# Kernel tuning notes

Measured on AMD Instinct MI355X. Metric: run time of the kernel, lower is better.

## Reference

```python
import jax, jax.numpy as jnp
import numpy as np

N_HEADS = 16

def setup_inputs() -> dict:
    key = jax.random.key(0)
    ks = jax.random.split(key, 5)
    B, T, D, L = 2, 2048, 1024, 128
    x = jax.random.normal(ks[0], (B, T, D), dtype=jnp.float32)
    w_q = jax.random.normal(ks[1], (D, D), dtype=jnp.float32) / np.sqrt(D)
    w_d = jax.random.normal(ks[2], (D, L), dtype=jnp.float32) / np.sqrt(D)
    w_k = jax.random.normal(ks[3], (L, D), dtype=jnp.float32) / np.sqrt(L)
    w_v = jax.random.normal(ks[4], (L, D), dtype=jnp.float32) / np.sqrt(L)
    mask = jnp.ones((B, T), dtype=jnp.int32)
    return {"x": x, "mask": mask, "w_q": w_q, "w_d": w_d, "w_k": w_k, "w_v": w_v}


def reference(x, mask, w_q, w_d, w_k, w_v):
    B, T, D = x.shape
    H = N_HEADS
    dh = D // H
    q = x @ w_q                      # [B,T,D]
    latent = x @ w_d                 # [B,T,L]
    k = latent @ w_k                 # [B,T,D]
    v = latent @ w_v                 # [B,T,D]

    def split(t):
        return t.reshape(B, T, H, dh).transpose(0, 2, 1, 3)  # [B,H,T,dh]

    q, k, v = split(q), split(k), split(v)
    scores = jnp.einsum('bhqd,bhkd->bhqk', q, k) / jnp.sqrt(jnp.float32(dh))
    causal = jnp.tril(jnp.ones((T, T), dtype=bool))          # [T,T]
    keep = causal[None, None, :, :] & (mask[:, None, None, :] != 0)
    scores = jnp.where(keep, scores, jnp.float32(-jnp.inf))
    probs = jax.nn.softmax(scores, axis=-1)
    out = jnp.einsum('bhqk,bhkd->bhqd', probs, v)            # [B,H,T,dh]
    return out.transpose(0, 2, 1, 3).reshape(B, T, D)
```

## Files before the change

kernel.cpp:

```cpp
#include <hip/hip_runtime.h>

typedef __attribute__((ext_vector_type(8))) short bf16x8;
typedef __attribute__((ext_vector_type(4))) float f32x4;
typedef __attribute__((ext_vector_type(4))) unsigned u32x4;

__device__ inline unsigned short f2bf(float f) {
  unsigned u = __builtin_bit_cast(unsigned, f);
  unsigned r = u + 0x7FFFu + ((u >> 16) & 1u);
  return (unsigned short)(r >> 16);
}
__device__ inline float bf2f(unsigned short s) {
  unsigned u = ((unsigned)s) << 16;
  return __builtin_bit_cast(float, u);
}
__device__ inline float fexp2(float x) { return __builtin_amdgcn_exp2f(x); }

__device__ inline void gload_lds16(const unsigned short* g, unsigned short* l) {
  __builtin_amdgcn_global_load_lds(
      (const __attribute__((address_space(1))) unsigned int*)g,
      (__attribute__((address_space(3))) unsigned int*)l, 16, 0, 0);
}

__device__ __host__ inline int pv_perm(int k) {
  return ((k >> 5) & 1) * 32 + ((k >> 2) & 3) * 8 + ((k >> 4) & 1) * 4 + (k & 3);
}

__global__ __launch_bounds__(256) void prep_kernel(
    const float* __restrict__ x, const int* __restrict__ mask,
    const float* __restrict__ w_q, const float* __restrict__ w_d,
    const float* __restrict__ w_k, const float* __restrict__ w_v,
    unsigned short* __restrict__ x_bf, unsigned short* __restrict__ wqdt,
    unsigned short* __restrict__ wkvt, float* __restrict__ bias,
    int* __restrict__ tileok) {
  int bid = blockIdx.x;
  if (bid < 1024) {
    int base = bid * 4096 + threadIdx.x * 4;
#pragma unroll
    for (int it = 0; it < 4; ++it) {
      int idx = base + it * 1024;
      float4 v = *(const float4*)&x[idx];
      ushort4 o;
      o.x = f2bf(v.x); o.y = f2bf(v.y); o.z = f2bf(v.z); o.w = f2bf(v.w);
      *(ushort4*)&x_bf[idx] = o;
    }
    return;
  }
  int tb = bid - 1024;
  if (tb >= 1408) {
    int i = (tb - 1408) * 256 + threadIdx.x;
    int mv = mask[i];
    bias[i] = mv ? 0.0f : -1e30f;
    int ok = __all(mv != 0);
    if ((threadIdx.x & 63) == 0) tileok[i >> 6] = ok;
    return;
  }
  const float* in; unsigned short* out; int R, C, tr, tc;
  if (tb < 1024)      { in = w_q; out = wqdt;               R = 1024; C = 1024; tr = tb >> 5; tc = tb & 31; }
  else if (tb < 1152) { int t2 = tb - 1024; in = w_d; out = wqdt + 1024 * 1024; R = 1024; C = 128; tr = t2 >> 2; tc = t2 & 3; }
  else if (tb < 1280) { int t2 = tb - 1152; in = w_k; out = wkvt;               R = 128; C = 1024; tr = t2 >> 5; tc = t2 & 31; }
  else                { int t2 = tb - 1280; in = w_v; out = wkvt + 1024 * 128;  R = 128; C = 1024; tr = t2 >> 5; tc = t2 & 31; }
  __shared__ float t[32][33];
  int r0 = tr * 32, c0 = tc * 32;
  int tx = threadIdx.x & 31, ty = threadIdx.x >> 5;
  for (int r = ty; r < 32; r += 8)
    t[r][tx] = in[(size_t)(r0 + r) * C + c0 + tx];
  __syncthreads();
  for (int cc = ty; cc < 32; cc += 8)
    out[(size_t)(c0 + cc) * R + r0 + tx] = f2bf(t[tx][cc]);
}

__global__ __launch_bounds__(256) void vt_kernel(const unsigned short* __restrict__ kv,
                                                 unsigned short* __restrict__ vt) {
  int bh = blockIdx.x, tt = blockIdx.y, dt = blockIdx.z;
  int b = bh >> 4, h = bh & 15;
  __shared__ unsigned short tile[32][33];
  int tx = threadIdx.x & 31, ty = threadIdx.x >> 5;
  for (int r = ty; r < 32; r += 8)
    tile[r][tx] = kv[(size_t)(b * 2048 + tt * 32 + r) * 2048 + 1024 + h * 64 + dt * 32 + tx];
  __syncthreads();
  int tile64 = tt >> 1;
  int wbase = (tt & 1) * 32;
  for (int r = ty; r < 32; r += 8) {
    int kp = pv_perm(wbase + tx);
    vt[((size_t)(bh * 64 + dt * 32 + r)) * 2048 + tile64 * 64 + kp] = tile[tx][r];
  }
}

template <int BN>
__global__ __launch_bounds__(256) void gemm_bt(const unsigned short* __restrict__ A, int lda,
                                               const unsigned short* __restrict__ Bt, int ldb,
                                               unsigned short* __restrict__ C, int ldc,
                                               int K) {
  constexpr int WM = (BN == 128) ? 2 : 4;
  constexpr int WN = 4 / WM;
  constexpr int MR = 128 / WM / 16;
  constexpr int NR = BN / WN / 16;
  constexpr int RPW = 128 / WM;
  constexpr int CPW = BN / WN;
  __shared__ unsigned short As[128 * 32];
  __shared__ unsigned short Bs[BN * 32];
  int m0 = blockIdx.x * 128, n0 = blockIdx.y * BN;
  int tid = threadIdx.x, w = tid >> 6, l = tid & 63;
  int lr = l & 15, lg = l >> 4;
  int wr = w / WN, wc = w % WN;
  f32x4 acc[MR][NR] = {};

  for (int k0 = 0; k0 < K; k0 += 32) {
    __syncthreads();
#pragma unroll
    for (int it = 0; it < 2; ++it) {
      int c = w * 2 + it;
      int row = c * 16 + (l >> 2);
      int col = (l & 3) * 8;
      gload_lds16(&A[(size_t)(m0 + row) * lda + k0 + col], &As[c * 512 + l * 8]);
    }
    if constexpr (BN == 128) {
#pragma unroll
      for (int it = 0; it < 2; ++it) {
        int c = w * 2 + it;
        int row = c * 16 + (l >> 2);
        int col = (l & 3) * 8;
        gload_lds16(&Bt[(size_t)(n0 + row) * ldb + k0 + col], &Bs[c * 512 + l * 8]);
      }
    } else {
      int row = w * 16 + (l >> 2);
      int col = (l & 3) * 8;
      gload_lds16(&Bt[(size_t)(n0 + row) * ldb + k0 + col], &Bs[w * 512 + l * 8]);
    }
    __syncthreads();
    bf16x8 af[MR], bfr[NR];
#pragma unroll
    for (int m = 0; m < MR; ++m)
      af[m] = *(const bf16x8*)&As[(wr * RPW + m * 16 + lr) * 32 + lg * 8];
#pragma unroll
    for (int n = 0; n < NR; ++n)
      bfr[n] = *(const bf16x8*)&Bs[(wc * CPW + n * 16 + lr) * 32 + lg * 8];
    __builtin_amdgcn_s_setprio(1);
#pragma unroll
    for (int m = 0; m < MR; ++m)
#pragma unroll
      for (int n = 0; n < NR; ++n)
        acc[m][n] = __builtin_amdgcn_mfma_f32_16x16x32_bf16(af[m], bfr[n], acc[m][n], 0, 0, 0);
    __builtin_amdgcn_s_setprio(0);
  }

#pragma unroll
  for (int m = 0; m < MR; ++m)
#pragma unroll
    for (int n = 0; n < NR; ++n)
#pragma unroll
      for (int i = 0; i < 4; ++i)
        C[(size_t)(m0 + wr * RPW + m * 16 + lg * 4 + i) * ldc + n0 + wc * CPW + n * 16 + lr] =
            f2bf(acc[m][n][i]);
}

__global__ __launch_bounds__(128, 4) void attn_kernel(const unsigned short* __restrict__ qg,
                                                      const unsigned short* __restrict__ kvg,
                                                      const unsigned short* __restrict__ vtg,
                                                      const float* __restrict__ biasg,
                                                      const int* __restrict__ tileokg,
                                                      float* __restrict__ outg) {
  const int bh = blockIdx.x, qt32 = 63 - blockIdx.y;
  const int b = bh >> 4, h = bh & 15;
  const int tid = threadIdx.x, w = tid >> 6, l = tid & 63;
  const int lr = l & 15, lg = l >> 4;

  __shared__ unsigned short Ks[64 * 72];
  __shared__ unsigned short Vs[64 * 72];

  const int qrow0 = qt32 * 32 + w * 16;
  const int nkv = (qt32 >> 1) + 1;
  const int diagoff = (qt32 & 1) * 32 + w * 16 + lr;
  const float QSCALE = 0.125f * 1.44269504089f;

  bf16x8 qf[2];
#pragma unroll
  for (int s = 0; s < 2; ++s) {
    bf16x8 raw = *(const bf16x8*)&qg[(size_t)(b * 2048 + qrow0 + lr) * 1152 + h * 64 + s * 32 + lg * 8];
#pragma unroll
    for (int j = 0; j < 8; ++j)
      raw[j] = (short)f2bf(bf2f((unsigned short)raw[j]) * QSCALE);
    qf[s] = raw;
  }

  f32x4 acc[4] = {};
  float m_i = -1e30f;
  float l_part = 0.f;

  bf16x8 kreg[4], vreg[4];
#pragma unroll
  for (int it = 0; it < 4; ++it) {
    int slot = it * 128 + tid, row = slot >> 3, c8 = (slot & 7) * 8;
    kreg[it] = *(const bf16x8*)&kvg[(size_t)(b * 2048 + row) * 2048 + h * 64 + c8];
    vreg[it] = *(const bf16x8*)&vtg[((size_t)(bh * 64 + row)) * 2048 + c8];
  }
#pragma unroll
  for (int it = 0; it < 4; ++it) {
    int slot = it * 128 + tid, row = slot >> 3, c8 = (slot & 7) * 8;
    *(bf16x8*)&Ks[row * 72 + c8] = kreg[it];
    *(bf16x8*)&Vs[row * 72 + c8] = vreg[it];
  }
  __syncthreads();

  for (int kt = 0; kt < nkv; ++kt) {
    if (kt + 1 < nkv) {
#pragma unroll
      for (int it = 0; it < 4; ++it) {
        int slot = it * 128 + tid, row = slot >> 3, c8 = (slot & 7) * 8;
        kreg[it] = *(const bf16x8*)&kvg[(size_t)(b * 2048 + (kt + 1) * 64 + row) * 2048 + h * 64 + c8];
        vreg[it] = *(const bf16x8*)&vtg[((size_t)(bh * 64 + row)) * 2048 + (kt + 1) * 64 + c8];
      }
    }

    f32x4 s[4];
    __builtin_amdgcn_s_setprio(1);
#pragma unroll
    for (int n = 0; n < 4; ++n) {
      f32x4 z = {};
#pragma unroll
      for (int ks = 0; ks < 2; ++ks) {
        bf16x8 kf = *(const bf16x8*)&Ks[(n * 16 + lr) * 72 + ks * 32 + lg * 8];
        z = __builtin_amdgcn_mfma_f32_16x16x32_bf16(kf, qf[ks], z, 0, 0, 0);
      }
      s[n] = z;
    }
    __builtin_amdgcn_s_setprio(0);

    const int tok = tileokg[b * 32 + kt];
    const bool diag = (kt == nkv - 1);
    float p[4][4];
    float mx = -1e30f;
    if (tok) {
      if (diag) {
#pragma unroll
        for (int n = 0; n < 4; ++n)
#pragma unroll
          for (int i = 0; i < 4; ++i) {
            float v = (n * 16 + lg * 4 + i <= diagoff) ? s[n][i] : -1e30f;
            p[n][i] = v;
            mx = fmaxf(mx, v);
          }
      } else {
#pragma unroll
        for (int n = 0; n < 4; ++n)
#pragma unroll
          for (int i = 0; i < 4; ++i) {
            p[n][i] = s[n][i];
            mx = fmaxf(mx, s[n][i]);
          }
      }
    } else {
#pragma unroll
      for (int n = 0; n < 4; ++n)
#pragma unroll
        for (int i = 0; i < 4; ++i) {
          int keyl = n * 16 + lg * 4 + i;
          float v = s[n][i] + biasg[b * 2048 + kt * 64 + keyl];
          if (diag) v = (keyl <= diagoff) ? v : -1e30f;
          p[n][i] = v;
          mx = fmaxf(mx, v);
        }
    }
    mx = fmaxf(mx, __shfl_xor(mx, 16, 64));
    mx = fmaxf(mx, __shfl_xor(mx, 32, 64));

    if (__any(mx - m_i > 8.0f)) {
      float mn = fmaxf(m_i, mx);
      float sc = fexp2(m_i - mn);
      m_i = mn;
      l_part *= sc;
      float scb[4];
#pragma unroll
      for (int i = 0; i < 4; ++i) scb[i] = __shfl(sc, lg * 4 + i, 64);
#pragma unroll
      for (int dt = 0; dt < 4; ++dt)
#pragma unroll
        for (int i = 0; i < 4; ++i) acc[dt][i] *= scb[i];
    }

    float rs = 0.f;
#pragma unroll
    for (int n = 0; n < 4; ++n)
#pragma unroll
      for (int i = 0; i < 4; ++i) {
        float e = fexp2(p[n][i] - m_i);
        p[n][i] = e;
        rs += e;
      }
    l_part += rs;

    unsigned pk[4][2];
#pragma unroll
    for (int n = 0; n < 4; ++n) {
      asm("v_cvt_pk_bf16_f32 %0, %1, %2" : "=v"(pk[n][0]) : "v"(p[n][0]), "v"(p[n][1]));
      asm("v_cvt_pk_bf16_f32 %0, %1, %2" : "=v"(pk[n][1]) : "v"(p[n][2]), "v"(p[n][3]));
    }
    bf16x8 paf[2];
#pragma unroll
    for (int ks = 0; ks < 2; ++ks) {
      u32x4 uv;
      uv[0] = pk[2 * ks][0];
      uv[1] = pk[2 * ks][1];
      uv[2] = pk[2 * ks + 1][0];
      uv[3] = pk[2 * ks + 1][1];
      paf[ks] = __builtin_bit_cast(bf16x8, uv);
    }

    __builtin_amdgcn_s_setprio(1);
#pragma unroll
    for (int ks = 0; ks < 2; ++ks) {
#pragma unroll
      for (int dt = 0; dt < 4; ++dt) {
        bf16x8 vf = *(const bf16x8*)&Vs[(dt * 16 + lr) * 72 + ks * 32 + lg * 8];
        acc[dt] = __builtin_amdgcn_mfma_f32_16x16x32_bf16(paf[ks], vf, acc[dt], 0, 0, 0);
      }
    }
    __builtin_amdgcn_s_setprio(0);

    __syncthreads();
    if (kt + 1 < nkv) {
#pragma unroll
      for (int it = 0; it < 4; ++it) {
        int slot = it * 128 + tid, row = slot >> 3, c8 = (slot & 7) * 8;
        *(bf16x8*)&Ks[row * 72 + c8] = kreg[it];
        *(bf16x8*)&Vs[row * 72 + c8] = vreg[it];
      }
      __syncthreads();
    }
  }

  float lt = l_part;
  lt += __shfl_xor(lt, 16, 64);
  lt += __shfl_xor(lt, 32, 64);
  float inv = 1.f / lt;
  float invb[4];
#pragma unroll
  for (int i = 0; i < 4; ++i) invb[i] = __shfl(inv, lg * 4 + i, 64);
#pragma unroll
  for (int dt = 0; dt < 4; ++dt)
#pragma unroll
    for (int i = 0; i < 4; ++i)
      outg[(size_t)(b * 2048 + qrow0 + lg * 4 + i) * 1024 + h * 64 + dt * 16 + lr] =
          acc[dt][i] * invb[i];
}

extern "C" void kernel_launch(void* const* d_in, const int* in_sizes, int n_in,
                              void* d_out, int out_size, void* d_ws, size_t ws_size,
                              hipStream_t stream) {
  const float* x    = (const float*)d_in[0];
  const int*   mask = (const int*)d_in[1];
  const float* w_q  = (const float*)d_in[2];
  const float* w_d  = (const float*)d_in[3];
  const float* w_k  = (const float*)d_in[4];
  const float* w_v  = (const float*)d_in[5];
  float* out = (float*)d_out;

  char* ws = (char*)d_ws;
  size_t off = 0;
  auto alloc = [&](size_t elems) {
    unsigned short* p = (unsigned short*)(ws + off);
    off += ((elems * 2 + 255) & ~(size_t)255);
    return p;
  };
  unsigned short* x_bf = alloc(4194304);
  unsigned short* wqdt = alloc(1152 * 1024);
  unsigned short* wkvt = alloc(2048 * 128);
  unsigned short* qlat = alloc(4096 * 1152);
  unsigned short* kv   = alloc(4096 * 2048);
  unsigned short* vt   = alloc(4194304);
  float* bias = (float*)alloc(8192);
  int* tileok = (int*)alloc(128);

  prep_kernel<<<2448, 256, 0, stream>>>(x, mask, w_q, w_d, w_k, w_v, x_bf, wqdt, wkvt, bias, tileok);

  gemm_bt<64><<<dim3(32, 18), 256, 0, stream>>>(x_bf, 1024, wqdt, 1024, qlat, 1152, 1024);
  gemm_bt<128><<<dim3(32, 16), 256, 0, stream>>>(qlat + 1024, 1152, wkvt, 128, kv, 2048, 128);

  vt_kernel<<<dim3(32, 64, 2), 256, 0, stream>>>(kv, vt);
  attn_kernel<<<dim3(32, 64), 128, 0, stream>>>(qlat, kv, vt, bias, tileok, out);
}
```

Before: 89.08 us.

## Fuse V transpose into KV GEMM epilogue and restructure attention to single-wave register tiles

Removes the separate vt_kernel by having a new gemm_kv kernel write K normally and V directly in the permuted transposed layout from its epilogue, saving a launch and a round trip of V through memory. The attention kernel becomes one wave per block handling 32 query rows as two 16-row sub-blocks. K/V fragments are loaded straight from global memory into registers with prefetch, dropping the LDS staging and __syncthreads. This raises register pressure and exposes global load latency in exchange for no LDS traffic or barriers, with fewer waves per block.

```diff
diff --git a/kernel.cpp b/kernel.cpp
--- a/kernel.cpp
+++ b/kernel.cpp
@@ -67,23 +67,6 @@
   __syncthreads();
   for (int cc = ty; cc < 32; cc += 8)
     out[(size_t)(c0 + cc) * R + r0 + tx] = f2bf(t[tx][cc]);
-}
-
-__global__ __launch_bounds__(256) void vt_kernel(const unsigned short* __restrict__ kv,
-                                                 unsigned short* __restrict__ vt) {
-  int bh = blockIdx.x, tt = blockIdx.y, dt = blockIdx.z;
-  int b = bh >> 4, h = bh & 15;
-  __shared__ unsigned short tile[32][33];
-  int tx = threadIdx.x & 31, ty = threadIdx.x >> 5;
-  for (int r = ty; r < 32; r += 8)
-    tile[r][tx] = kv[(size_t)(b * 2048 + tt * 32 + r) * 2048 + 1024 + h * 64 + dt * 32 + tx];
-  __syncthreads();
-  int tile64 = tt >> 1;
-  int wbase = (tt & 1) * 32;
-  for (int r = ty; r < 32; r += 8) {
-    int kp = pv_perm(wbase + tx);
-    vt[((size_t)(bh * 64 + dt * 32 + r)) * 2048 + tile64 * 64 + kp] = tile[tx][r];
-  }
 }
 
 template <int BN>
@@ -154,100 +137,163 @@
             f2bf(acc[m][n][i]);
 }
 
-__global__ __launch_bounds__(128, 4) void attn_kernel(const unsigned short* __restrict__ qg,
-                                                      const unsigned short* __restrict__ kvg,
-                                                      const unsigned short* __restrict__ vtg,
-                                                      const float* __restrict__ biasg,
-                                                      const int* __restrict__ tileokg,
-                                                      float* __restrict__ outg) {
+__global__ __launch_bounds__(256) void gemm_kv(const unsigned short* __restrict__ A,
+                                               const unsigned short* __restrict__ Bt,
+                                               unsigned short* __restrict__ kvK,
+                                               unsigned short* __restrict__ vt) {
+  __shared__ unsigned short As[128 * 32];
+  __shared__ unsigned short Bs[128 * 32];
+  int m0 = blockIdx.x * 128, n0 = blockIdx.y * 128;
+  int tid = threadIdx.x, w = tid >> 6, l = tid & 63;
+  int lr = l & 15, lg = l >> 4;
+  int wr = w >> 1, wc = w & 1;
+  f32x4 acc[4][4] = {};
+
+  for (int k0 = 0; k0 < 128; k0 += 32) {
+    __syncthreads();
+#pragma unroll
+    for (int it = 0; it < 2; ++it) {
+      int c = w * 2 + it;
+      int row = c * 16 + (l >> 2);
+      int col = (l & 3) * 8;
+      gload_lds16(&A[(size_t)(m0 + row) * 1152 + k0 + col], &As[c * 512 + l * 8]);
+      gload_lds16(&Bt[(size_t)(n0 + row) * 128 + k0 + col], &Bs[c * 512 + l * 8]);
+    }
+    __syncthreads();
+    bf16x8 af[4], bfr[4];
+#pragma unroll
+    for (int m = 0; m < 4; ++m)
+      af[m] = *(const bf16x8*)&As[(wr * 64 + m * 16 + lr) * 32 + lg * 8];
+#pragma unroll
+    for (int n = 0; n < 4; ++n)
+      bfr[n] = *(const bf16x8*)&Bs[(wc * 64 + n * 16 + lr) * 32 + lg * 8];
+    __builtin_amdgcn_s_setprio(1);
+#pragma unroll
+    for (int m = 0; m < 4; ++m)
+#pragma unroll
+      for (int n = 0; n < 4; ++n)
+        acc[m][n] = __builtin_amdgcn_mfma_f32_16x16x32_bf16(af[m], bfr[n], acc[m][n], 0, 0, 0);
+    __builtin_amdgcn_s_setprio(0);
+  }
+
+  if (blockIdx.y < 8) {
+#pragma unroll
+    for (int m = 0; m < 4; ++m)
+#pragma unroll
+      for (int n = 0; n < 4; ++n)
+#pragma unroll
+        for (int i = 0; i < 4; ++i)
+          kvK[(size_t)(m0 + wr * 64 + m * 16 + lg * 4 + i) * 2048 + n0 + wc * 64 + n * 16 + lr] =
+              f2bf(acc[m][n][i]);
+  } else {
+#pragma unroll
+    for (int m = 0; m < 4; ++m)
+#pragma unroll
+      for (int n = 0; n < 4; ++n) {
+        int vc = n0 - 1024 + wc * 64 + n * 16 + lr;
+        int hh = vc >> 6, dd = vc & 63;
+        int row0 = m0 + wr * 64 + m * 16 + lg * 4;
+        int bb = row0 >> 11, t0 = row0 & 2047;
+        size_t vrow = (size_t)((bb * 16 + hh) * 64 + dd);
+        int slot = (t0 >> 6) * 64 + pv_perm(t0 & 63);
+        ushort4 o;
+        o.x = f2bf(acc[m][n][0]); o.y = f2bf(acc[m][n][1]);
+        o.z = f2bf(acc[m][n][2]); o.w = f2bf(acc[m][n][3]);
+        *(ushort4*)&vt[vrow * 2048 + slot] = o;
+      }
+  }
+}
+
+__global__ __launch_bounds__(64, 2) void attn_kernel(const unsigned short* __restrict__ qg,
+                                                     const unsigned short* __restrict__ kvg,
+                                                     const unsigned short* __restrict__ vtg,
+                                                     const float* __restrict__ biasg,
+                                                     const int* __restrict__ tileokg,
+                                                     float* __restrict__ outg) {
   const int bh = blockIdx.x, qt32 = 63 - blockIdx.y;
   const int b = bh >> 4, h = bh & 15;
-  const int tid = threadIdx.x, w = tid >> 6, l = tid & 63;
-  const int lr = l & 15, lg = l >> 4;
-
-  __shared__ unsigned short Ks[64 * 72];
-  __shared__ unsigned short Vs[64 * 72];
-
-  const int qrow0 = qt32 * 32 + w * 16;
+  const int l = threadIdx.x & 63, lr = l & 15, lg = l >> 4;
+  const int qrow0 = qt32 * 32;
   const int nkv = (qt32 >> 1) + 1;
-  const int diagoff = (qt32 & 1) * 32 + w * 16 + lr;
+  const int dov0 = (qt32 & 1) * 32 + lr;
   const float QSCALE = 0.125f * 1.44269504089f;
 
-  bf16x8 qf[2];
-#pragma unroll
-  for (int s = 0; s < 2; ++s) {
-    bf16x8 raw = *(const bf16x8*)&qg[(size_t)(b * 2048 + qrow0 + lr) * 1152 + h * 64 + s * 32 + lg * 8];
-#pragma unroll
-    for (int j = 0; j < 8; ++j)
-      raw[j] = (short)f2bf(bf2f((unsigned short)raw[j]) * QSCALE);
-    qf[s] = raw;
-  }
-
-  f32x4 acc[4] = {};
-  float m_i = -1e30f;
-  float l_part = 0.f;
-
-  bf16x8 kreg[4], vreg[4];
-#pragma unroll
-  for (int it = 0; it < 4; ++it) {
-    int slot = it * 128 + tid, row = slot >> 3, c8 = (slot & 7) * 8;
-    kreg[it] = *(const bf16x8*)&kvg[(size_t)(b * 2048 + row) * 2048 + h * 64 + c8];
-    vreg[it] = *(const bf16x8*)&vtg[((size_t)(bh * 64 + row)) * 2048 + c8];
-  }
-#pragma unroll
-  for (int it = 0; it < 4; ++it) {
-    int slot = it * 128 + tid, row = slot >> 3, c8 = (slot & 7) * 8;
-    *(bf16x8*)&Ks[row * 72 + c8] = kreg[it];
-    *(bf16x8*)&Vs[row * 72 + c8] = vreg[it];
-  }
-  __syncthreads();
+  bf16x8 qf[2][2];
+#pragma unroll
+  for (int qb = 0; qb < 2; ++qb)
+#pragma unroll
+    for (int ks = 0; ks < 2; ++ks) {
+      bf16x8 raw = *(const bf16x8*)&qg[(size_t)(b * 2048 + qrow0 + qb * 16 + lr) * 1152 +
+                                       h * 64 + ks * 32 + lg * 8];
+#pragma unroll
+      for (int j = 0; j < 8; ++j)
+        raw[j] = (short)f2bf(bf2f((unsigned short)raw[j]) * QSCALE);
+      qf[qb][ks] = raw;
+    }
+
+  const unsigned short* kptr = kvg + (size_t)(b * 2048 + lr) * 2048 + h * 64 + lg * 8;
+  const unsigned short* vptr = vtg + (size_t)(bh * 64 + lr) * 2048 + lg * 8;
+
+  bf16x8 kf[4][2], vf[4][2];
+#pragma unroll
+  for (int n = 0; n < 4; ++n)
+#pragma unroll
+    for (int ks = 0; ks < 2; ++ks) {
+      kf[n][ks] = *(const bf16x8*)(kptr + (size_t)(n * 16) * 2048 + ks * 32);
+      vf[n][ks] = *(const bf16x8*)(vptr + (size_t)(n * 16) * 2048 + ks * 32);
+    }
+
+  f32x4 acc[4][2] = {};
+  float m_i[2] = {-1e30f, -1e30f};
+  float l_part[2] = {0.f, 0.f};
 
   for (int kt = 0; kt < nkv; ++kt) {
+    f32x4 s[2][4];
+    __builtin_amdgcn_s_setprio(1);
+#pragma unroll
+    for (int qb = 0; qb < 2; ++qb)
+#pragma unroll
+      for (int n = 0; n < 4; ++n) {
+        f32x4 z = {};
+#pragma unroll
+        for (int ks = 0; ks < 2; ++ks)
+          z = __builtin_amdgcn_mfma_f32_16x16x32_bf16(kf[n][ks], qf[qb][ks], z, 0, 0, 0);
+        s[qb][n] = z;
+      }
+    __builtin_amdgcn_s_setprio(0);
+
     if (kt + 1 < nkv) {
 #pragma unroll
-      for (int it = 0; it < 4; ++it) {
-        int slot = it * 128 + tid, row = slot >> 3, c8 = (slot & 7) * 8;
-        kreg[it] = *(const bf16x8*)&kvg[(size_t)(b * 2048 + (kt + 1) * 64 + row) * 2048 + h * 64 + c8];
-        vreg[it] = *(const bf16x8*)&vtg[((size_t)(bh * 64 + row)) * 2048 + (kt + 1) * 64 + c8];
-      }
-    }
-
-    f32x4 s[4];
-    __builtin_amdgcn_s_setprio(1);
-#pragma unroll
-    for (int n = 0; n < 4; ++n) {
-      f32x4 z = {};
-#pragma unroll
-      for (int ks = 0; ks < 2; ++ks) {
-        bf16x8 kf = *(const bf16x8*)&Ks[(n * 16 + lr) * 72 + ks * 32 + lg * 8];
-        z = __builtin_amdgcn_mfma_f32_16x16x32_bf16(kf, qf[ks], z, 0, 0, 0);
-      }
-      s[n] = z;
-    }
-    __builtin_amdgcn_s_setprio(0);
+      for (int n = 0; n < 4; ++n)
+#pragma unroll
+        for (int ks = 0; ks < 2; ++ks)
+          kf[n][ks] = *(const bf16x8*)(kptr + (size_t)((kt + 1) * 64 + n * 16) * 2048 + ks * 32);
+    }
 
     const int tok = tileokg[b * 32 + kt];
     const bool diag = (kt == nkv - 1);
-    float p[4][4];
-    float mx = -1e30f;
+    float mx[2] = {-1e30f, -1e30f};
     if (tok) {
       if (diag) {
 #pragma unroll
-        for (int n = 0; n < 4; ++n)
-#pragma unroll
-          for (int i = 0; i < 4; ++i) {
-            float v = (n * 16 + lg * 4 + i <= diagoff) ? s[n][i] : -1e30f;
-            p[n][i] = v;
-            mx = fmaxf(mx, v);
-          }
+        for (int qb = 0; qb < 2; ++qb)
+#pragma unroll
+          for (int n = 0; n < 4; ++n)
+#pragma unroll
+            for (int i = 0; i < 4; ++i) {
+              int keyl = n * 16 + lg * 4 + i;
+              float v = (keyl <= dov0 + qb * 16) ? s[qb][n][i] : -1e30f;
+              s[qb][n][i] = v;
+              mx[qb] = fmaxf(mx[qb], v);
+            }
       } else {
 #pragma unroll
-        for (int n = 0; n < 4; ++n)
-#pragma unroll
-          for (int i = 0; i < 4; ++i) {
-            p[n][i] = s[n][i];
-            mx = fmaxf(mx, s[n][i]);
-          }
+        for (int qb = 0; qb < 2; ++qb)
+#pragma unroll
+          for (int n = 0; n < 4; ++n)
+#pragma unroll
+            for (int i = 0; i < 4; ++i)
+              mx[qb] = fmaxf(mx[qb], s[qb][n][i]);
       }
     } else {
 #pragma unroll
@@ -255,93 +301,104 @@
 #pragma unroll
         for (int i = 0; i < 4; ++i) {
           int keyl = n * 16 + lg * 4 + i;
-          float v = s[n][i] + biasg[b * 2048 + kt * 64 + keyl];
-          if (diag) v = (keyl <= diagoff) ? v : -1e30f;
-          p[n][i] = v;
-          mx = fmaxf(mx, v);
+          float bsv = biasg[b * 2048 + kt * 64 + keyl];
+#pragma unroll
+          for (int qb = 0; qb < 2; ++qb) {
+            float v = s[qb][n][i] + bsv;
+            if (diag) v = (keyl <= dov0 + qb * 16) ? v : -1e30f;
+            s[qb][n][i] = v;
+            mx[qb] = fmaxf(mx[qb], v);
+          }
         }
     }
-    mx = fmaxf(mx, __shfl_xor(mx, 16, 64));
-    mx = fmaxf(mx, __shfl_xor(mx, 32, 64));
-
-    if (__any(mx - m_i > 8.0f)) {
-      float mn = fmaxf(m_i, mx);
-      float sc = fexp2(m_i - mn);
-      m_i = mn;
-      l_part *= sc;
-      float scb[4];
-#pragma unroll
-      for (int i = 0; i < 4; ++i) scb[i] = __shfl(sc, lg * 4 + i, 64);
+#pragma unroll
+    for (int qb = 0; qb < 2; ++qb) {
+      mx[qb] = fmaxf(mx[qb], __shfl_xor(mx[qb], 16, 64));
+      mx[qb] = fmaxf(mx[qb], __shfl_xor(mx[qb], 32, 64));
+    }
+
+    float g = fmaxf(mx[0] - m_i[0], mx[1] - m_i[1]);
+    if (__any(g > 8.0f)) {
+#pragma unroll
+      for (int qb = 0; qb < 2; ++qb) {
+        float mn = fmaxf(m_i[qb], mx[qb]);
+        float sc = fexp2(m_i[qb] - mn);
+        m_i[qb] = mn;
+        l_part[qb] *= sc;
+        float scb[4];
+#pragma unroll
+        for (int i = 0; i < 4; ++i) scb[i] = __shfl(sc, lg * 4 + i, 64);
+#pragma unroll
+        for (int dt = 0; dt < 4; ++dt)
+#pragma unroll
+          for (int i = 0; i < 4; ++i) acc[dt][qb][i] *= scb[i];
+      }
+    }
+
+#pragma unroll
+    for (int qb = 0; qb < 2; ++qb) {
+      float rs = 0.f;
+#pragma unroll
+      for (int n = 0; n < 4; ++n)
+#pragma unroll
+        for (int i = 0; i < 4; ++i) {
+          float e = fexp2(s[qb][n][i] - m_i[qb]);
+          s[qb][n][i] = e;
+          rs += e;
+        }
+      l_part[qb] += rs;
+    }
+
+    bf16x8 paf[2][2];
+#pragma unroll
+    for (int qb = 0; qb < 2; ++qb)
+#pragma unroll
+      for (int ks = 0; ks < 2; ++ks) {
+        unsigned t0, t1, t2, t3;
+        asm("v_cvt_pk_bf16_f32 %0, %1, %2" : "=v"(t0) : "v"(s[qb][2 * ks][0]), "v"(s[qb][2 * ks][1]));
+        asm("v_cvt_pk_bf16_f32 %0, %1, %2" : "=v"(t1) : "v"(s[qb][2 * ks][2]), "v"(s[qb][2 * ks][3]));
+        asm("v_cvt_pk_bf16_f32 %0, %1, %2" : "=v"(t2) : "v"(s[qb][2 * ks + 1][0]), "v"(s[qb][2 * ks + 1][1]));
+        asm("v_cvt_pk_bf16_f32 %0, %1, %2" : "=v"(t3) : "v"(s[qb][2 * ks + 1][2]), "v"(s[qb][2 * ks + 1][3]));
+        u32x4 uv;
+        uv[0] = t0; uv[1] = t1; uv[2] = t2; uv[3] = t3;
+        paf[qb][ks] = __builtin_bit_cast(bf16x8, uv);
+      }
+
+    __builtin_amdgcn_s_setprio(1);
+#pragma unroll
+    for (int ks = 0; ks < 2; ++ks)
 #pragma unroll
       for (int dt = 0; dt < 4; ++dt)
 #pragma unroll
-        for (int i = 0; i < 4; ++i) acc[dt][i] *= scb[i];
-    }
-
-    float rs = 0.f;
-#pragma unroll
-    for (int n = 0; n < 4; ++n)
-#pragma unroll
-      for (int i = 0; i < 4; ++i) {
-        float e = fexp2(p[n][i] - m_i);
-        p[n][i] = e;
-        rs += e;
-      }
-    l_part += rs;
-
-    unsigned pk[4][2];
-#pragma unroll
-    for (int n = 0; n < 4; ++n) {
-      asm("v_cvt_pk_bf16_f32 %0, %1, %2" : "=v"(pk[n][0]) : "v"(p[n][0]), "v"(p[n][1]));
-      asm("v_cvt_pk_bf16_f32 %0, %1, %2" : "=v"(pk[n][1]) : "v"(p[n][2]), "v"(p[n][3]));
-    }
-    bf16x8 paf[2];
-#pragma unroll
-    for (int ks = 0; ks < 2; ++ks) {
-      u32x4 uv;
-      uv[0] = pk[2 * ks][0];
-      uv[1] = pk[2 * ks][1];
-      uv[2] = pk[2 * ks + 1][0];
-      uv[3] = pk[2 * ks + 1][1];
-      paf[ks] = __builtin_bit_cast(bf16x8, uv);
-    }
-
-    __builtin_amdgcn_s_setprio(1);
-#pragma unroll
-    for (int ks = 0; ks < 2; ++ks) {
-#pragma unroll
-      for (int dt = 0; dt < 4; ++dt) {
-        bf16x8 vf = *(const bf16x8*)&Vs[(dt * 16 + lr) * 72 + ks * 32 + lg * 8];
-        acc[dt] = __builtin_amdgcn_mfma_f32_16x16x32_bf16(paf[ks], vf, acc[dt], 0, 0, 0);
-      }
-    }
+        for (int qb = 0; qb < 2; ++qb)
+          acc[dt][qb] = __builtin_amdgcn_mfma_f32_16x16x32_bf16(paf[qb][ks], vf[dt][ks], acc[dt][qb], 0, 0, 0);
     __builtin_amdgcn_s_setprio(0);
 
-    __syncthreads();
     if (kt + 1 < nkv) {
 #pragma unroll
-      for (int it = 0; it < 4; ++it) {
-        int slot = it * 128 + tid, row = slot >> 3, c8 = (slot & 7) * 8;
-        *(bf16x8*)&Ks[row * 72 + c8] = kreg[it];
-        *(bf16x8*)&Vs[row * 72 + c8] = vreg[it];
-      }
-      __syncthreads();
-    }
-  }
-
-  float lt = l_part;
-  lt += __shfl_xor(lt, 16, 64);
-  lt += __shfl_xor(lt, 32, 64);
-  float inv = 1.f / lt;
-  float invb[4];
-#pragma unroll
-  for (int i = 0; i < 4; ++i) invb[i] = __shfl(inv, lg * 4 + i, 64);
-#pragma unroll
-  for (int dt = 0; dt < 4; ++dt)
-#pragma unroll
-    for (int i = 0; i < 4; ++i)
-      outg[(size_t)(b * 2048 + qrow0 + lg * 4 + i) * 1024 + h * 64 + dt * 16 + lr] =
-          acc[dt][i] * invb[i];
+      for (int dt = 0; dt < 4; ++dt)
+#pragma unroll
+        for (int ks = 0; ks < 2; ++ks)
+          vf[dt][ks] = *(const bf16x8*)(vptr + (size_t)(dt * 16) * 2048 + (kt + 1) * 64 + ks * 32);
+    }
+  }
+
+#pragma unroll
+  for (int qb = 0; qb < 2; ++qb) {
+    float lt = l_part[qb];
+    lt += __shfl_xor(lt, 16, 64);
+    lt += __shfl_xor(lt, 32, 64);
+    float inv = 1.f / lt;
+    float invb[4];
+#pragma unroll
+    for (int i = 0; i < 4; ++i) invb[i] = __shfl(inv, lg * 4 + i, 64);
+#pragma unroll
+    for (int dt = 0; dt < 4; ++dt)
+#pragma unroll
+      for (int i = 0; i < 4; ++i)
+        outg[(size_t)(b * 2048 + qrow0 + qb * 16 + lg * 4 + i) * 1024 + h * 64 + dt * 16 + lr] =
+            acc[dt][qb][i] * invb[i];
+  }
 }
 
 extern "C" void kernel_launch(void* const* d_in, const int* in_sizes, int n_in,
@@ -374,8 +431,7 @@
   prep_kernel<<<2448, 256, 0, stream>>>(x, mask, w_q, w_d, w_k, w_v, x_bf, wqdt, wkvt, bias, tileok);
 
   gemm_bt<64><<<dim3(32, 18), 256, 0, stream>>>(x_bf, 1024, wqdt, 1024, qlat, 1152, 1024);
-  gemm_bt<128><<<dim3(32, 16), 256, 0, stream>>>(qlat + 1024, 1152, wkvt, 128, kv, 2048, 128);
-
-  vt_kernel<<<dim3(32, 64, 2), 256, 0, stream>>>(kv, vt);
-  attn_kernel<<<dim3(32, 64), 128, 0, stream>>>(qlat, kv, vt, bias, tileok, out);
-}
+  gemm_kv<<<dim3(32, 16), 256, 0, stream>>>(qlat + 1024, wkvt, kv, vt);
+
+  attn_kernel<<<dim3(32, 64), 64, 0, stream>>>(qlat, kv, vt, bias, tileok, out);
+}
```

After: 112.0 us. 1.26x slower.

## Split attention KV range into chunks with reduce pass; fuse V transpose into GEMM

Applied to the files above, without the earlier changes.

Attention now splits long causal query tiles into up to four KV chunks of eight tiles each, writing unnormalized partial outputs plus row max and sum to a workspace. A new reduce kernel combines them with log-sum-exp rescaling. This is meant to balance the uneven causal workload and raise parallelism. Separately, the K/V projection GEMM writes V directly in the permuted transposed layout, removing the separate vt_kernel launch. In exchange it adds partial-buffer traffic and an extra reduce launch.

```diff
diff --git a/kernel.cpp b/kernel.cpp
--- a/kernel.cpp
+++ b/kernel.cpp
@@ -67,23 +67,6 @@
   __syncthreads();
   for (int cc = ty; cc < 32; cc += 8)
     out[(size_t)(c0 + cc) * R + r0 + tx] = f2bf(t[tx][cc]);
-}
-
-__global__ __launch_bounds__(256) void vt_kernel(const unsigned short* __restrict__ kv,
-                                                 unsigned short* __restrict__ vt) {
-  int bh = blockIdx.x, tt = blockIdx.y, dt = blockIdx.z;
-  int b = bh >> 4, h = bh & 15;
-  __shared__ unsigned short tile[32][33];
-  int tx = threadIdx.x & 31, ty = threadIdx.x >> 5;
-  for (int r = ty; r < 32; r += 8)
-    tile[r][tx] = kv[(size_t)(b * 2048 + tt * 32 + r) * 2048 + 1024 + h * 64 + dt * 32 + tx];
-  __syncthreads();
-  int tile64 = tt >> 1;
-  int wbase = (tt & 1) * 32;
-  for (int r = ty; r < 32; r += 8) {
-    int kp = pv_perm(wbase + tx);
-    vt[((size_t)(bh * 64 + dt * 32 + r)) * 2048 + tile64 * 64 + kp] = tile[tx][r];
-  }
 }
 
 template <int BN>
@@ -154,13 +137,91 @@
             f2bf(acc[m][n][i]);
 }
 
+__global__ __launch_bounds__(256) void gemm_kv(const unsigned short* __restrict__ A,
+                                               const unsigned short* __restrict__ Bt,
+                                               unsigned short* __restrict__ kvK,
+                                               unsigned short* __restrict__ vt) {
+  __shared__ unsigned short As[128 * 32];
+  __shared__ unsigned short Bs[128 * 32];
+  int m0 = blockIdx.x * 128, n0 = blockIdx.y * 128;
+  int tid = threadIdx.x, w = tid >> 6, l = tid & 63;
+  int lr = l & 15, lg = l >> 4;
+  int wr = w >> 1, wc = w & 1;
+  f32x4 acc[4][4] = {};
+
+  for (int k0 = 0; k0 < 128; k0 += 32) {
+    __syncthreads();
+#pragma unroll
+    for (int it = 0; it < 2; ++it) {
+      int c = w * 2 + it;
+      int row = c * 16 + (l >> 2);
+      int col = (l & 3) * 8;
+      gload_lds16(&A[(size_t)(m0 + row) * 1152 + k0 + col], &As[c * 512 + l * 8]);
+      gload_lds16(&Bt[(size_t)(n0 + row) * 128 + k0 + col], &Bs[c * 512 + l * 8]);
+    }
+    __syncthreads();
+    bf16x8 af[4], bfr[4];
+#pragma unroll
+    for (int m = 0; m < 4; ++m)
+      af[m] = *(const bf16x8*)&As[(wr * 64 + m * 16 + lr) * 32 + lg * 8];
+#pragma unroll
+    for (int n = 0; n < 4; ++n)
+      bfr[n] = *(const bf16x8*)&Bs[(wc * 64 + n * 16 + lr) * 32 + lg * 8];
+    __builtin_amdgcn_s_setprio(1);
+#pragma unroll
+    for (int m = 0; m < 4; ++m)
+#pragma unroll
+      for (int n = 0; n < 4; ++n)
+        acc[m][n] = __builtin_amdgcn_mfma_f32_16x16x32_bf16(af[m], bfr[n], acc[m][n], 0, 0, 0);
+    __builtin_amdgcn_s_setprio(0);
+  }
+
+  if (blockIdx.y < 8) {
+#pragma unroll
+    for (int m = 0; m < 4; ++m)
+#pragma unroll
+      for (int n = 0; n < 4; ++n)
+#pragma unroll
+        for (int i = 0; i < 4; ++i)
+          kvK[(size_t)(m0 + wr * 64 + m * 16 + lg * 4 + i) * 2048 + n0 + wc * 64 + n * 16 + lr] =
+              f2bf(acc[m][n][i]);
+  } else {
+#pragma unroll
+    for (int m = 0; m < 4; ++m)
+#pragma unroll
+      for (int n = 0; n < 4; ++n) {
+        int vc = n0 - 1024 + wc * 64 + n * 16 + lr;
+        int hh = vc >> 6, dd = vc & 63;
+        int row0 = m0 + wr * 64 + m * 16 + lg * 4;
+        int bb = row0 >> 11, t0 = row0 & 2047;
+        size_t vrow = (size_t)((bb * 16 + hh) * 64 + dd);
+        int slot = (t0 >> 6) * 64 + pv_perm(t0 & 63);
+        ushort4 o;
+        o.x = f2bf(acc[m][n][0]); o.y = f2bf(acc[m][n][1]);
+        o.z = f2bf(acc[m][n][2]); o.w = f2bf(acc[m][n][3]);
+        *(ushort4*)&vt[vrow * 2048 + slot] = o;
+      }
+  }
+}
+
+#define PSTRIDE 2112
 __global__ __launch_bounds__(128, 4) void attn_kernel(const unsigned short* __restrict__ qg,
                                                       const unsigned short* __restrict__ kvg,
                                                       const unsigned short* __restrict__ vtg,
                                                       const float* __restrict__ biasg,
                                                       const int* __restrict__ tileokg,
-                                                      float* __restrict__ outg) {
-  const int bh = blockIdx.x, qt32 = 63 - blockIdx.y;
+                                                      float* __restrict__ partg) {
+  const int bh = blockIdx.x;
+  const int y2 = 159 - blockIdx.y;
+  int qt32, c;
+  if (y2 < 16)      { qt32 = y2; c = 0; }
+  else if (y2 < 48) { int t = y2 - 16; qt32 = 16 + (t >> 1); c = t & 1; }
+  else if (y2 < 96) { int t = y2 - 48; qt32 = 32 + t / 3; c = t - (t / 3) * 3; }
+  else              { int t = y2 - 96; qt32 = 48 + (t >> 2); c = t & 3; }
+  const int nkv = (qt32 >> 1) + 1;
+  const int k0t = c * 8;
+  const int kend = min(nkv, k0t + 8);
+
   const int b = bh >> 4, h = bh & 15;
   const int tid = threadIdx.x, w = tid >> 6, l = tid & 63;
   const int lr = l & 15, lg = l >> 4;
@@ -169,7 +230,6 @@
   __shared__ unsigned short Vs[64 * 72];
 
   const int qrow0 = qt32 * 32 + w * 16;
-  const int nkv = (qt32 >> 1) + 1;
   const int diagoff = (qt32 & 1) * 32 + w * 16 + lr;
   const float QSCALE = 0.125f * 1.44269504089f;
 
@@ -191,8 +251,8 @@
 #pragma unroll
   for (int it = 0; it < 4; ++it) {
     int slot = it * 128 + tid, row = slot >> 3, c8 = (slot & 7) * 8;
-    kreg[it] = *(const bf16x8*)&kvg[(size_t)(b * 2048 + row) * 2048 + h * 64 + c8];
-    vreg[it] = *(const bf16x8*)&vtg[((size_t)(bh * 64 + row)) * 2048 + c8];
+    kreg[it] = *(const bf16x8*)&kvg[(size_t)(b * 2048 + k0t * 64 + row) * 2048 + h * 64 + c8];
+    vreg[it] = *(const bf16x8*)&vtg[((size_t)(bh * 64 + row)) * 2048 + k0t * 64 + c8];
   }
 #pragma unroll
   for (int it = 0; it < 4; ++it) {
@@ -202,8 +262,8 @@
   }
   __syncthreads();
 
-  for (int kt = 0; kt < nkv; ++kt) {
-    if (kt + 1 < nkv) {
+  for (int kt = k0t; kt < kend; ++kt) {
+    if (kt + 1 < kend) {
 #pragma unroll
       for (int it = 0; it < 4; ++it) {
         int slot = it * 128 + tid, row = slot >> 3, c8 = (slot & 7) * 8;
@@ -308,17 +368,16 @@
 
     __builtin_amdgcn_s_setprio(1);
 #pragma unroll
-    for (int ks = 0; ks < 2; ++ks) {
+    for (int ks = 0; ks < 2; ++ks)
 #pragma unroll
       for (int dt = 0; dt < 4; ++dt) {
         bf16x8 vf = *(const bf16x8*)&Vs[(dt * 16 + lr) * 72 + ks * 32 + lg * 8];
         acc[dt] = __builtin_amdgcn_mfma_f32_16x16x32_bf16(paf[ks], vf, acc[dt], 0, 0, 0);
       }
-    }
     __builtin_amdgcn_s_setprio(0);
 
     __syncthreads();
-    if (kt + 1 < nkv) {
+    if (kt + 1 < kend) {
 #pragma unroll
       for (int it = 0; it < 4; ++it) {
         int slot = it * 128 + tid, row = slot >> 3, c8 = (slot & 7) * 8;
@@ -332,16 +391,43 @@
   float lt = l_part;
   lt += __shfl_xor(lt, 16, 64);
   lt += __shfl_xor(lt, 32, 64);
-  float inv = 1.f / lt;
-  float invb[4];
-#pragma unroll
-  for (int i = 0; i < 4; ++i) invb[i] = __shfl(inv, lg * 4 + i, 64);
+  float* pb = partg + (size_t)(bh * 160 + y2) * PSTRIDE;
 #pragma unroll
   for (int dt = 0; dt < 4; ++dt)
 #pragma unroll
     for (int i = 0; i < 4; ++i)
-      outg[(size_t)(b * 2048 + qrow0 + lg * 4 + i) * 1024 + h * 64 + dt * 16 + lr] =
-          acc[dt][i] * invb[i];
+      pb[(w * 16 + lg * 4 + i) * 64 + dt * 16 + lr] = acc[dt][i];
+  if (lg == 0) {
+    pb[2048 + w * 16 + lr] = m_i;
+    pb[2048 + 32 + w * 16 + lr] = lt;
+  }
+}
+
+__global__ __launch_bounds__(256) void attn_reduce(const float* __restrict__ partg,
+                                                   float* __restrict__ outg) {
+  const int bh = blockIdx.x, qt32 = blockIdx.y;
+  const int b = bh >> 4, h = bh & 15;
+  const int d = threadIdx.x & 63, rg = threadIdx.x >> 6;
+  const int band = qt32 >> 4;
+  const int nch = band + 1;
+  int y2base;
+  if (band == 0)      y2base = qt32;
+  else if (band == 1) y2base = 16 + (qt32 - 16) * 2;
+  else if (band == 2) y2base = 48 + (qt32 - 32) * 3;
+  else                y2base = 96 + (qt32 - 48) * 4;
+  const float* p0 = partg + (size_t)(bh * 160 + y2base) * PSTRIDE;
+
+  for (int r = rg; r < 32; r += 4) {
+    float m = -1e30f;
+    for (int c = 0; c < nch; ++c) m = fmaxf(m, p0[c * PSTRIDE + 2048 + r]);
+    float osum = 0.f, lsum = 0.f;
+    for (int c = 0; c < nch; ++c) {
+      float wgt = fexp2(p0[c * PSTRIDE + 2048 + r] - m);
+      lsum += wgt * p0[c * PSTRIDE + 2048 + 32 + r];
+      osum += wgt * p0[c * PSTRIDE + r * 64 + d];
+    }
+    outg[(size_t)(b * 2048 + qt32 * 32 + r) * 1024 + h * 64 + d] = osum / lsum;
+  }
 }
 
 extern "C" void kernel_launch(void* const* d_in, const int* in_sizes, int n_in,
@@ -370,12 +456,13 @@
   unsigned short* vt   = alloc(4194304);
   float* bias = (float*)alloc(8192);
   int* tileok = (int*)alloc(128);
+  float* part = (float*)alloc((size_t)32 * 160 * PSTRIDE * 2);
 
   prep_kernel<<<2448, 256, 0, stream>>>(x, mask, w_q, w_d, w_k, w_v, x_bf, wqdt, wkvt, bias, tileok);
 
   gemm_bt<64><<<dim3(32, 18), 256, 0, stream>>>(x_bf, 1024, wqdt, 1024, qlat, 1152, 1024);
-  gemm_bt<128><<<dim3(32, 16), 256, 0, stream>>>(qlat + 1024, 1152, wkvt, 128, kv, 2048, 128);
-
-  vt_kernel<<<dim3(32, 64, 2), 256, 0, stream>>>(kv, vt);
-  attn_kernel<<<dim3(32, 64), 128, 0, stream>>>(qlat, kv, vt, bias, tileok, out);
-}
+  gemm_kv<<<dim3(32, 16), 256, 0, stream>>>(qlat + 1024, wkvt, kv, vt);
+
+  attn_kernel<<<dim3(32, 160), 128, 0, stream>>>(qlat, kv, vt, bias, tileok, part);
+  attn_reduce<<<dim3(32, 64), 256, 0, stream>>>(part, out);
+}
```

Result: slower. 103.2 us (+15.9%).
